# Optimization experiments

Hardware: AMD Instinct MI355X
Metric: run time of the kernel (lower is better)

The kernel has to match this reference:

```python
import jax, jax.numpy as jnp
import numpy as np
from jax.ops import segment_sum

N = 100000   # total nodes
M = 50000    # propagated subset size (len(index))
E = 600000   # edges over the subset graph
D = 128      # embedding_size
EPS = 1e-8
N_LAYERS = 3  # self.LayerNums


def setup_inputs() -> dict:
    key = jax.random.key(0)
    ks = jax.random.split(key, 12)
    features = jax.random.normal(ks[0], (N, D), dtype=jnp.float32)
    index = jnp.arange(M, dtype=jnp.int64)  # subset of nodes that get propagated
    edge_row = jax.random.randint(ks[1], (E,), 0, M, dtype=jnp.int64)
    edge_col = jax.random.randint(ks[2], (E,), 0, M, dtype=jnp.int64)
    edge_val = jax.random.uniform(ks[3], (E,), dtype=jnp.float32)
    # MLP prediction weights: D -> D//2 -> D//4 -> D//6 -> 1 (last no bias)
    def xavier(k, fan_in, fan_out):
        lim = jnp.sqrt(6.0 / (fan_in + fan_out)).astype(jnp.float32)
        return jax.random.uniform(k, (fan_in, fan_out), jnp.float32, -lim, lim)
    W1 = xavier(ks[4], D, D // 2); b1 = jnp.zeros((D // 2,), jnp.float32)
    W2 = xavier(ks[5], D // 2, D // 4); b2 = jnp.zeros((D // 4,), jnp.float32)
    W3 = xavier(ks[6], D // 4, D // 6); b3 = jnp.zeros((D // 6,), jnp.float32)
    W4 = xavier(ks[7], D // 6, 1)
    return {"features": features, "index": index, "edge_row": edge_row,
            "edge_col": edge_col, "edge_val": edge_val,
            "W1": W1, "b1": b1, "W2": W2, "b2": b2, "W3": W3, "b3": b3, "W4": W4}


def _gcn_layer(features, index, row, col, val):
    # symmetric normalization: d = rowsum(A)+eps; A' = d^-1/2 A d^-1/2
    deg = segment_sum(val, row, num_segments=M)
    d_inv_sqrt = jax.lax.rsqrt(deg + EPS)
    nval = val * d_inv_sqrt[row] * d_inv_sqrt[col]
    sub = features[index]                      # [M, D] subset_features
    msg = sub[col] * nval[:, None]             # [E, D]
    out = segment_sum(msg, row, num_segments=M)  # spmm -> [M, D]
    # new_features[index] = out; untouched rows keep original features
    return features.at[index].set(out)


def reference(features, index, edge_row, edge_col, edge_val,
              W1, b1, W2, b2, W3, b3, W4):
    x = features
    for _ in range(N_LAYERS):
        x = _gcn_layer(x, index, edge_row, edge_col, edge_val)
    # MLP prediction head (eval mode: dropout off), LeakyReLU slope 0.01
    h = jax.nn.leaky_relu(x @ W1 + b1, 0.01)
    h = jax.nn.leaky_relu(h @ W2 + b2, 0.01)
    h = jax.nn.leaky_relu(h @ W3 + b3, 0.01)
    return jax.nn.sigmoid(h @ W4)              # [N, 1]
```

## Files before the change

kernel.cpp:

```cpp
#include <hip/hip_runtime.h>
#include <math.h>

#define NN 100000
#define MM 50000
#define EE 600000
#define DD 128
#define NB 196
#define NNP 100096
#define EE4 750000

typedef short bf16x8 __attribute__((ext_vector_type(8)));
typedef float f32x4 __attribute__((ext_vector_type(4)));

__device__ __forceinline__ float bl(unsigned u) { return __uint_as_float(u << 16); }
__device__ __forceinline__ float bh(unsigned u) { return __uint_as_float(u & 0xFFFF0000u); }
__device__ __forceinline__ unsigned rne(float f) {
    unsigned u = __float_as_uint(f);
    return (u + 0x7FFFu + ((u >> 16) & 1u)) >> 16;
}
__device__ __forceinline__ unsigned pk2(float a, float b) { return rne(a) | (rne(b) << 16); }

__device__ __forceinline__ void fma21(float h, const float* wrow, float* a) {
    #pragma unroll
    for (int j = 0; j < 21; ++j) a[j] = fmaf(h, wrow[j], a[j]);
}

__global__ __launch_bounds__(256) void front_kernel(
    const int* __restrict__ row, const float* __restrict__ val,
    unsigned long long* __restrict__ dcpack, int* __restrict__ slot,
    const float* __restrict__ feat, const int* __restrict__ index,
    unsigned* __restrict__ X0b, unsigned* __restrict__ Xfull,
    const float* __restrict__ W1, const float* __restrict__ W2,
    unsigned* __restrict__ W1b, unsigned* __restrict__ W2b) {
    int i = blockIdx.x * 256 + threadIdx.x;
    int n = i >> 6, u = i & 63;
    {
        float2 f = ((const float2*)feat)[(size_t)n * 64 + u];
        Xfull[(size_t)n * 64 + u] = pk2(f.x, f.y);
    }
    if (i < MM * 64) {
        int idx = index[n];
        float2 f = ((const float2*)feat)[(size_t)idx * 64 + u];
        X0b[((size_t)(u >> 4) * MM + n) * 16 + (u & 15)] = pk2(f.x, f.y);
    }
    if (i < 4096) {
        int j = i >> 6, kp = i & 63;
        W1b[i] = pk2(W1[(2 * kp) * 64 + j], W1[(2 * kp + 1) * 64 + j]);
    } else if (i < 5120) {
        int t = i - 4096;
        int j = t >> 5, kp = t & 31;
        W2b[t] = pk2(W2[(2 * kp) * 32 + j], W2[(2 * kp + 1) * 32 + j]);
    }
    if (i < EE) {
        int r = row[i];
        unsigned long long add = (1ULL << 44) | (unsigned long long)(val[i] * 4294967296.0f);
        unsigned long long old = atomicAdd(&dcpack[r], add);
        slot[i] = (int)(old >> 44);
    }
}

__global__ void setup_kernel(const unsigned long long* __restrict__ dcpack,
                             float* __restrict__ dis, int* __restrict__ cnt,
                             int* __restrict__ blockhist) {
    __shared__ int lh[256];
    int tid = threadIdx.x;
    int i = blockIdx.x * 256 + tid;
    lh[tid] = 0;
    __syncthreads();
    if (i < MM) {
        unsigned long long pkv = dcpack[i];
        int v = (int)(pkv >> 44);
        float dsum = (float)(pkv & ((1ULL << 44) - 1)) * (1.0f / 4294967296.0f);
        dis[i] = rsqrtf(dsum + 1e-8f);
        cnt[i] = v;
        atomicAdd(&lh[min(v, 255)], 1);
    }
    __syncthreads();
    blockhist[tid * NB + blockIdx.x] = lh[tid];
}

__global__ void scan_kernel(const int* __restrict__ blockhist,
                            int* __restrict__ blockoff, int* __restrict__ total) {
    int d = blockIdx.x;
    int lane = threadIdx.x;
    int carry = 0;
    for (int base = 0; base < NB; base += 64) {
        int b = base + lane;
        int v = (b < NB) ? blockhist[d * NB + b] : 0;
        int x = v;
        #pragma unroll
        for (int off = 1; off < 64; off <<= 1) {
            int t = __shfl_up(x, off, 64);
            if (lane >= off) x += t;
        }
        if (b < NB) blockoff[d * NB + b] = carry + x - v;
        carry += __shfl(x, 63);
    }
    if (lane == 0) total[d] = carry;
}

__global__ void sort_kernel(const int* __restrict__ cnt, const int* __restrict__ blockoff,
                            const int* __restrict__ total, const int* __restrict__ index,
                            int4* __restrict__ meta, int* __restrict__ row_s4,
                            int2* __restrict__ cv_s) {
    __shared__ int lh[256], sbin[256], spad[256], ws[8];
    int tid = threadIdx.x, lane = tid & 63, w = tid >> 6;
    lh[tid] = 0;
    int t = total[tid];
    int v1 = t, v2 = t * ((tid + 3) & ~3);
    int x1 = v1, x2 = v2;
    #pragma unroll
    for (int off = 1; off < 64; off <<= 1) {
        int t1 = __shfl_up(x1, off, 64);
        int t2 = __shfl_up(x2, off, 64);
        if (lane >= off) { x1 += t1; x2 += t2; }
    }
    if (lane == 63) { ws[w] = x1; ws[4 + w] = x2; }
    __syncthreads();
    int a1 = 0, a2 = 0;
    for (int q = 0; q < w; ++q) { a1 += ws[q]; a2 += ws[4 + q]; }
    sbin[tid] = a1 + x1 - v1;
    spad[tid] = a2 + x2 - v2;
    __syncthreads();
    int i = blockIdx.x * 256 + tid;
    if (i < MM) {
        int d = cnt[i], c = min(d, 255);
        int lrank = atomicAdd(&lh[c], 1);
        int k = blockoff[c * NB + blockIdx.x] + lrank;
        int spos = sbin[c] + k;
        int s4 = spad[c] + k * ((d + 3) & ~3);
        meta[MM - 1 - spos] = make_int4(s4, d, i, index[i]);
        row_s4[i] = s4;
        int p4 = (d + 3) & ~3;
        for (int pp = d; pp < p4; ++pp) cv_s[s4 + pp] = make_int2(0, 0);
    }
}

__global__ void scatter_kernel(const int* __restrict__ row, const int* __restrict__ col,
                               const float* __restrict__ val, const float* __restrict__ dis,
                               const int* __restrict__ row_s4, const int* __restrict__ slot,
                               int2* __restrict__ cv_s) {
    int e = blockIdx.x * 256 + threadIdx.x;
    if (e < EE) {
        int r = row[e], c = col[e];
        int pos = row_s4[r] + slot[e];
        cv_s[pos] = make_int2(c, __float_as_int(val[e] * dis[r] * dis[c]));
    }
}

template <int TAG>
__global__ __launch_bounds__(256) void spmmq_kernel(
    const int4* __restrict__ meta, const int2* __restrict__ cv,
    const unsigned* __restrict__ X, unsigned* __restrict__ Y, int last) {
    int b = blockIdx.x;
    int xcd = b & 7;
    int q = xcd >> 1;
    int vb = ((b >> 3) << 1) + (xcd & 1);
    if (vb >= (MM + 15) / 16) return;
    int lane = threadIdx.x & 63, wid = threadIdx.x >> 6;
    int g = lane >> 4, sub = lane & 15;
    int ri = vb * 16 + wid * 4 + g;
    bool valid = (ri < MM);
    int rc = valid ? ri : (MM - 1);
    int4 mt = meta[rc];
    int s = mt.x, d = mt.y;
    const uint4* __restrict__ CV = (const uint4*)cv;
    const unsigned* __restrict__ Xq = X + (size_t)q * (MM * 16);
    float a0 = 0.f, a1 = 0.f;
    int e4 = s + d;
    for (int base = s; base < e4; base += 4) {
        uint4 p0 = CV[(base >> 1)];
        uint4 p1 = CV[(base >> 1) + 1];
        unsigned u0 = Xq[(int)p0.x * 16 + sub];
        unsigned u1 = Xq[(int)p0.z * 16 + sub];
        unsigned u2 = Xq[(int)p1.x * 16 + sub];
        unsigned u3 = Xq[(int)p1.z * 16 + sub];
        float v0 = __uint_as_float(p0.y), v1 = __uint_as_float(p0.w);
        float v2 = __uint_as_float(p1.y), v3 = __uint_as_float(p1.w);
        a0 = fmaf(v0, bl(u0), a0); a1 = fmaf(v0, bh(u0), a1);
        a0 = fmaf(v1, bl(u1), a0); a1 = fmaf(v1, bh(u1), a1);
        a0 = fmaf(v2, bl(u2), a0); a1 = fmaf(v2, bh(u2), a1);
        a0 = fmaf(v3, bl(u3), a0); a1 = fmaf(v3, bh(u3), a1);
    }
    if (valid) {
        unsigned o = pk2(a0, a1);
        if (last) Y[(size_t)mt.w * 64 + q * 16 + sub] = o;
        else      Y[(size_t)q * (MM * 16) + (size_t)mt.z * 16 + sub] = o;
    }
}

__global__ __launch_bounds__(256) void mlp_kernel(
    const unsigned* __restrict__ Xfull,
    const unsigned* __restrict__ W1b, const float* __restrict__ b1,
    const unsigned* __restrict__ W2b, const float* __restrict__ b2,
    const float* __restrict__ W3, const float* __restrict__ b3,
    const float* __restrict__ W4, float* __restrict__ out) {
    __shared__ float hls[4 * 1088];
    int tid = threadIdx.x;
    int lane = tid & 63, w = tid >> 6;
    int p = lane & 15, q = lane >> 4;
    float* hw = hls + w * 1088;
    int nb = blockIdx.x * 64;
    int node = nb + w * 16 + p;

    bf16x8 af[4];
    #pragma unroll
    for (int kc = 0; kc < 4; ++kc) {
        uint4 u = *(const uint4*)(Xfull + (size_t)node * 64 + kc * 16 + q * 4);
        af[kc] = *(const bf16x8*)&u;
    }
    f32x4 acc[4];
    #pragma unroll
    for (int jt = 0; jt < 4; ++jt) {
        float bv = b1[jt * 16 + p];
        acc[jt][0] = bv; acc[jt][1] = bv; acc[jt][2] = bv; acc[jt][3] = bv;
    }
    #pragma unroll
    for (int jt = 0; jt < 4; ++jt) {
        #pragma unroll
        for (int kc = 0; kc < 4; ++kc) {
            uint4 u = *(const uint4*)(W1b + (jt * 16 + p) * 64 + kc * 16 + q * 4);
            bf16x8 bf = *(const bf16x8*)&u;
            acc[jt] = __builtin_amdgcn_mfma_f32_16x16x32_bf16(af[kc], bf, acc[jt], 0, 0, 0);
        }
    }
    #pragma unroll
    for (int jt = 0; jt < 4; ++jt) {
        #pragma unroll
        for (int r = 0; r < 4; ++r) {
            float v = acc[jt][r];
            v = v > 0.f ? v : 0.01f * v;
            hw[(q * 4 + r) * 68 + jt * 16 + p] = v;
        }
    }
    bf16x8 a2f[2];
    #pragma unroll
    for (int kc = 0; kc < 2; ++kc) {
        const float* hp = hw + p * 68 + kc * 32 + q * 8;
        f32x4 v0 = *(const f32x4*)hp;
        f32x4 v1 = *(const f32x4*)(hp + 4);
        uint4 uu = make_uint4(pk2(v0[0], v0[1]), pk2(v0[2], v0[3]),
                              pk2(v1[0], v1[1]), pk2(v1[2], v1[3]));
        a2f[kc] = *(const bf16x8*)&uu;
    }
    f32x4 acc2[2];
    #pragma unroll
    for (int jt = 0; jt < 2; ++jt) {
        float bv = b2[jt * 16 + p];
        acc2[jt][0] = bv; acc2[jt][1] = bv; acc2[jt][2] = bv; acc2[jt][3] = bv;
        #pragma unroll
        for (int kc = 0; kc < 2; ++kc) {
            uint4 u = *(const uint4*)(W2b + (jt * 16 + p) * 32 + kc * 16 + q * 4);
            bf16x8 bf = *(const bf16x8*)&u;
            acc2[jt] = __builtin_amdgcn_mfma_f32_16x16x32_bf16(a2f[kc], bf, acc2[jt], 0, 0, 0);
        }
    }
    #pragma unroll
    for (int jt = 0; jt < 2; ++jt) {
        #pragma unroll
        for (int r = 0; r < 4; ++r) {
            float v = acc2[jt][r];
            v = v > 0.f ? v : 0.01f * v;
            hw[(q * 4 + r) * 36 + jt * 16 + p] = v;
        }
    }
    float a3[21];
    #pragma unroll
    for (int j = 0; j < 21; ++j) a3[j] = b3[j];
    #pragma unroll 4
    for (int k = 0; k < 32; ++k) {
        float hk = hw[p * 36 + k];
        fma21(hk, W3 + k * 21, a3);
    }
    float s = 0.f;
    #pragma unroll
    for (int j = 0; j < 21; ++j) {
        float vj = a3[j] > 0.f ? a3[j] : 0.01f * a3[j];
        s = fmaf(vj, W4[j], s);
    }
    if (q == 0) {
        int n = nb + w * 16 + p;
        if (n < NN) out[n] = 1.f / (1.f + expf(-s));
    }
}

extern "C" void kernel_launch(void* const* d_in, const int* in_sizes, int n_in,
                              void* d_out, int out_size, void* d_ws, size_t ws_size,
                              hipStream_t stream) {
    const float* feat = (const float*)d_in[0];
    const int*   index = (const int*)d_in[1];
    const int*   erow = (const int*)d_in[2];
    const int*   ecol = (const int*)d_in[3];
    const float* evalp = (const float*)d_in[4];
    const float* W1 = (const float*)d_in[5];
    const float* b1 = (const float*)d_in[6];
    const float* W2 = (const float*)d_in[7];
    const float* b2 = (const float*)d_in[8];
    const float* W3 = (const float*)d_in[9];
    const float* b3 = (const float*)d_in[10];
    const float* W4 = (const float*)d_in[11];
    float* out = (float*)d_out;

    char* ws = (char*)d_ws;
    size_t off = 0;
    auto alloc = [&](size_t bytes) -> void* {
        void* p = ws + off;
        off += (bytes + 255) & ~(size_t)255;
        return p;
    };
    unsigned long long* dcpack = (unsigned long long*)alloc((size_t)MM * 8);
    int2*  cv_s    = (int2*) alloc((size_t)EE4 * 8);
    float* dis     = (float*)alloc((size_t)MM * 4);
    int*   cnt     = (int*)  alloc((size_t)MM * 4);
    int*   slot    = (int*)  alloc((size_t)EE * 4);
    int*   row_s4  = (int*)  alloc((size_t)MM * 4);
    int*   blockhist = (int*)alloc((size_t)256 * NB * 4);
    int*   blockoff  = (int*)alloc((size_t)256 * NB * 4);
    int*   total     = (int*)alloc((size_t)256 * 4);
    int4*  meta      = (int4*)alloc((size_t)MM * 16);
    unsigned* W1b  = (unsigned*)alloc(4096 * 4);
    unsigned* W2b  = (unsigned*)alloc(1024 * 4);
    unsigned*       X0b   = (unsigned*)      alloc((size_t)MM * DD * 2);
    unsigned*       Xa    = (unsigned*)      alloc((size_t)MM * DD * 2);
    unsigned*       Xb    = (unsigned*)      alloc((size_t)MM * DD * 2);
    unsigned*       Xfull = (unsigned*)      alloc((size_t)NNP * DD * 2);

    hipMemsetAsync(dcpack, 0, (size_t)MM * 8, stream);

    front_kernel<<<(NN * 64) / 256, 256, 0, stream>>>(
        erow, evalp, dcpack, slot, feat, index, X0b, Xfull, W1, W2, W1b, W2b);
    setup_kernel<<<NB, 256, 0, stream>>>(dcpack, dis, cnt, blockhist);
    scan_kernel<<<256, 64, 0, stream>>>(blockhist, blockoff, total);
    sort_kernel<<<NB, 256, 0, stream>>>(cnt, blockoff, total, index, meta, row_s4, cv_s);
    scatter_kernel<<<(EE + 255) / 256, 256, 0, stream>>>(erow, ecol, evalp, dis,
                                                         row_s4, slot, cv_s);

    const int NGRID = (((MM + 15) / 16 + 1) / 2) * 8 + 8;
    spmmq_kernel<0><<<NGRID, 256, 0, stream>>>(meta, cv_s, X0b, Xa, 0);
    spmmq_kernel<1><<<NGRID, 256, 0, stream>>>(meta, cv_s, Xa, Xb, 0);
    spmmq_kernel<2><<<NGRID, 256, 0, stream>>>(meta, cv_s, Xb, Xfull, 1);

    mlp_kernel<<<(NNP + 63) / 64, 256, 0, stream>>>(Xfull, W1b, b1, W2b, b2,
                                                    W3, b3, W4, out);
}
```

Baseline: 273.6 us.

## Drop full-feature bf16 copy, split SpMM into per-quarter launches, gather via inverse index

Removes the Xfull bf16 copy of all N nodes. The MLP now reads propagated rows from the final quarter-split buffer through an inverse-index map, and untouched rows straight from fp32 features. Each SpMM layer is split into four launches, one per 32-column quarter, replacing the XCD-based block remapping so each launch's gather set stays cache-resident. Edge and output accesses use nontemporal loads and stores. This trades fewer bytes in the front kernel for 12 SpMM launches instead of 3 and a divergent gather path in the MLP.

```diff
diff --git a/kernel.cpp b/kernel.cpp
--- a/kernel.cpp
+++ b/kernel.cpp
@@ -11,6 +11,7 @@
 
 typedef short bf16x8 __attribute__((ext_vector_type(8)));
 typedef float f32x4 __attribute__((ext_vector_type(4)));
+typedef unsigned u32x4 __attribute__((ext_vector_type(4)));
 
 __device__ __forceinline__ float bl(unsigned u) { return __uint_as_float(u << 16); }
 __device__ __forceinline__ float bh(unsigned u) { return __uint_as_float(u & 0xFFFF0000u); }
@@ -26,23 +27,22 @@
 }
 
 __global__ __launch_bounds__(256) void front_kernel(
-    const int* __restrict__ row, const float* __restrict__ val,
+    const int* __restrict__ erow, const float* __restrict__ eval,
     unsigned long long* __restrict__ dcpack, int* __restrict__ slot,
     const float* __restrict__ feat, const int* __restrict__ index,
-    unsigned* __restrict__ X0b, unsigned* __restrict__ Xfull,
+    int* __restrict__ invidx1, unsigned* __restrict__ X0q,
     const float* __restrict__ W1, const float* __restrict__ W2,
     unsigned* __restrict__ W1b, unsigned* __restrict__ W2b) {
     int i = blockIdx.x * 256 + threadIdx.x;
-    int n = i >> 6, u = i & 63;
+    int n = i >> 5, u = i & 31;
     {
-        float2 f = ((const float2*)feat)[(size_t)n * 64 + u];
-        Xfull[(size_t)n * 64 + u] = pk2(f.x, f.y);
-    }
-    if (i < MM * 64) {
         int idx = index[n];
-        float2 f = ((const float2*)feat)[(size_t)idx * 64 + u];
-        X0b[((size_t)(u >> 4) * MM + n) * 16 + (u & 15)] = pk2(f.x, f.y);
-    }
+        float4 f = ((const float4*)feat)[(size_t)idx * 32 + u];
+        unsigned* dst = X0q + (size_t)(u >> 3) * (MM * 16) + n * 16 + ((2 * u) & 15);
+        dst[0] = pk2(f.x, f.y);
+        dst[1] = pk2(f.z, f.w);
+    }
+    if (i < MM) invidx1[index[i]] = i + 1;
     if (i < 4096) {
         int j = i >> 6, kp = i & 63;
         W1b[i] = pk2(W1[(2 * kp) * 64 + j], W1[(2 * kp + 1) * 64 + j]);
@@ -52,8 +52,8 @@
         W2b[t] = pk2(W2[(2 * kp) * 32 + j], W2[(2 * kp + 1) * 32 + j]);
     }
     if (i < EE) {
-        int r = row[i];
-        unsigned long long add = (1ULL << 44) | (unsigned long long)(val[i] * 4294967296.0f);
+        int r = erow[i];
+        unsigned long long add = (1ULL << 44) | (unsigned long long)(eval[i] * 4294967296.0f);
         unsigned long long old = atomicAdd(&dcpack[r], add);
         slot[i] = (int)(old >> 44);
     }
@@ -100,7 +100,7 @@
 }
 
 __global__ void sort_kernel(const int* __restrict__ cnt, const int* __restrict__ blockoff,
-                            const int* __restrict__ total, const int* __restrict__ index,
+                            const int* __restrict__ total,
                             int4* __restrict__ meta, int* __restrict__ row_s4,
                             int2* __restrict__ cv_s) {
     __shared__ int lh[256], sbin[256], spad[256], ws[8];
@@ -129,7 +129,7 @@
         int k = blockoff[c * NB + blockIdx.x] + lrank;
         int spos = sbin[c] + k;
         int s4 = spad[c] + k * ((d + 3) & ~3);
-        meta[MM - 1 - spos] = make_int4(s4, d, i, index[i]);
+        meta[MM - 1 - spos] = make_int4(s4, d, i, 0);
         row_s4[i] = s4;
         int p4 = (d + 3) & ~3;
         for (int pp = d; pp < p4; ++pp) cv_s[s4 + pp] = make_int2(0, 0);
@@ -148,29 +148,22 @@
     }
 }
 
-template <int TAG>
 __global__ __launch_bounds__(256) void spmmq_kernel(
     const int4* __restrict__ meta, const int2* __restrict__ cv,
-    const unsigned* __restrict__ X, unsigned* __restrict__ Y, int last) {
-    int b = blockIdx.x;
-    int xcd = b & 7;
-    int q = xcd >> 1;
-    int vb = ((b >> 3) << 1) + (xcd & 1);
-    if (vb >= (MM + 15) / 16) return;
+    const unsigned* __restrict__ Xq, unsigned* __restrict__ Yq) {
     int lane = threadIdx.x & 63, wid = threadIdx.x >> 6;
     int g = lane >> 4, sub = lane & 15;
-    int ri = vb * 16 + wid * 4 + g;
+    int ri = blockIdx.x * 16 + wid * 4 + g;
     bool valid = (ri < MM);
     int rc = valid ? ri : (MM - 1);
     int4 mt = meta[rc];
     int s = mt.x, d = mt.y;
-    const uint4* __restrict__ CV = (const uint4*)cv;
-    const unsigned* __restrict__ Xq = X + (size_t)q * (MM * 16);
+    const u32x4* __restrict__ CV = (const u32x4*)cv;
     float a0 = 0.f, a1 = 0.f;
     int e4 = s + d;
     for (int base = s; base < e4; base += 4) {
-        uint4 p0 = CV[(base >> 1)];
-        uint4 p1 = CV[(base >> 1) + 1];
+        u32x4 p0 = __builtin_nontemporal_load(CV + (base >> 1));
+        u32x4 p1 = __builtin_nontemporal_load(CV + (base >> 1) + 1);
         unsigned u0 = Xq[(int)p0.x * 16 + sub];
         unsigned u1 = Xq[(int)p0.z * 16 + sub];
         unsigned u2 = Xq[(int)p1.x * 16 + sub];
@@ -183,14 +176,13 @@
         a0 = fmaf(v3, bl(u3), a0); a1 = fmaf(v3, bh(u3), a1);
     }
     if (valid) {
-        unsigned o = pk2(a0, a1);
-        if (last) Y[(size_t)mt.w * 64 + q * 16 + sub] = o;
-        else      Y[(size_t)q * (MM * 16) + (size_t)mt.z * 16 + sub] = o;
+        __builtin_nontemporal_store(pk2(a0, a1), Yq + mt.z * 16 + sub);
     }
 }
 
 __global__ __launch_bounds__(256) void mlp_kernel(
-    const unsigned* __restrict__ Xfull,
+    const unsigned* __restrict__ Xc, const float* __restrict__ feat,
+    const int* __restrict__ invidx1,
     const unsigned* __restrict__ W1b, const float* __restrict__ b1,
     const unsigned* __restrict__ W2b, const float* __restrict__ b2,
     const float* __restrict__ W3, const float* __restrict__ b3,
@@ -202,12 +194,27 @@
     float* hw = hls + w * 1088;
     int nb = blockIdx.x * 64;
     int node = nb + w * 16 + p;
+    int nc = min(node, NN - 1);
+    int iv = invidx1[nc];
 
     bf16x8 af[4];
-    #pragma unroll
-    for (int kc = 0; kc < 4; ++kc) {
-        uint4 u = *(const uint4*)(Xfull + (size_t)node * 64 + kc * 16 + q * 4);
-        af[kc] = *(const bf16x8*)&u;
+    if (iv > 0) {
+        int r = iv - 1;
+        #pragma unroll
+        for (int kc = 0; kc < 4; ++kc) {
+            uint4 u = *(const uint4*)(Xc + (size_t)kc * (MM * 16) + r * 16 + q * 4);
+            af[kc] = *(const bf16x8*)&u;
+        }
+    } else {
+        const float4* F = (const float4*)feat;
+        #pragma unroll
+        for (int kc = 0; kc < 4; ++kc) {
+            float4 f0 = F[(size_t)nc * 32 + kc * 8 + q * 2];
+            float4 f1 = F[(size_t)nc * 32 + kc * 8 + q * 2 + 1];
+            uint4 uu = make_uint4(pk2(f0.x, f0.y), pk2(f0.z, f0.w),
+                                  pk2(f1.x, f1.y), pk2(f1.z, f1.w));
+            af[kc] = *(const bf16x8*)&uu;
+        }
     }
     f32x4 acc[4];
     #pragma unroll
@@ -279,8 +286,7 @@
         s = fmaf(vj, W4[j], s);
     }
     if (q == 0) {
-        int n = nb + w * 16 + p;
-        if (n < NN) out[n] = 1.f / (1.f + expf(-s));
+        if (node < NN) out[node] = 1.f / (1.f + expf(-s));
     }
 }
 
@@ -309,6 +315,9 @@
         return p;
     };
     unsigned long long* dcpack = (unsigned long long*)alloc((size_t)MM * 8);
+    int*   invidx1 = (int*)  alloc((size_t)NN * 4);
+    size_t zero_span = (size_t)((char*)invidx1 - (char*)dcpack) + (size_t)NN * 4;
+
     int2*  cv_s    = (int2*) alloc((size_t)EE4 * 8);
     float* dis     = (float*)alloc((size_t)MM * 4);
     int*   cnt     = (int*)  alloc((size_t)MM * 4);
@@ -320,26 +329,35 @@
     int4*  meta      = (int4*)alloc((size_t)MM * 16);
     unsigned* W1b  = (unsigned*)alloc(4096 * 4);
     unsigned* W2b  = (unsigned*)alloc(1024 * 4);
-    unsigned*       X0b   = (unsigned*)      alloc((size_t)MM * DD * 2);
-    unsigned*       Xa    = (unsigned*)      alloc((size_t)MM * DD * 2);
-    unsigned*       Xb    = (unsigned*)      alloc((size_t)MM * DD * 2);
-    unsigned*       Xfull = (unsigned*)      alloc((size_t)NNP * DD * 2);
-
-    hipMemsetAsync(dcpack, 0, (size_t)MM * 8, stream);
-
-    front_kernel<<<(NN * 64) / 256, 256, 0, stream>>>(
-        erow, evalp, dcpack, slot, feat, index, X0b, Xfull, W1, W2, W1b, W2b);
+    unsigned* X0q  = (unsigned*)alloc((size_t)MM * DD * 2);
+    unsigned* Xa   = (unsigned*)alloc((size_t)MM * DD * 2);
+    unsigned* Xb   = (unsigned*)alloc((size_t)MM * DD * 2);
+    unsigned* Xc   = (unsigned*)alloc((size_t)MM * DD * 2);
+
+    (void)hipMemsetAsync(dcpack, 0, zero_span, stream);
+
+    front_kernel<<<(MM * 32) / 256, 256, 0, stream>>>(
+        erow, evalp, dcpack, slot, feat, index, invidx1, X0q, W1, W2, W1b, W2b);
     setup_kernel<<<NB, 256, 0, stream>>>(dcpack, dis, cnt, blockhist);
     scan_kernel<<<256, 64, 0, stream>>>(blockhist, blockoff, total);
-    sort_kernel<<<NB, 256, 0, stream>>>(cnt, blockoff, total, index, meta, row_s4, cv_s);
+    sort_kernel<<<NB, 256, 0, stream>>>(cnt, blockoff, total, meta, row_s4, cv_s);
     scatter_kernel<<<(EE + 255) / 256, 256, 0, stream>>>(erow, ecol, evalp, dis,
                                                          row_s4, slot, cv_s);
 
-    const int NGRID = (((MM + 15) / 16 + 1) / 2) * 8 + 8;
-    spmmq_kernel<0><<<NGRID, 256, 0, stream>>>(meta, cv_s, X0b, Xa, 0);
-    spmmq_kernel<1><<<NGRID, 256, 0, stream>>>(meta, cv_s, Xa, Xb, 0);
-    spmmq_kernel<2><<<NGRID, 256, 0, stream>>>(meta, cv_s, Xb, Xfull, 1);
-
-    mlp_kernel<<<(NNP + 63) / 64, 256, 0, stream>>>(Xfull, W1b, b1, W2b, b2,
+    const int QSTRIDE = MM * 16;
+    const int SPGRID = (MM + 15) / 16;
+    unsigned* bufs[4] = { X0q, Xa, Xb, Xc };
+    for (int layer = 0; layer < 3; ++layer) {
+        const unsigned* Xs = bufs[layer];
+        unsigned* Yd = bufs[layer + 1];
+        for (int q = 0; q < 4; ++q) {
+            spmmq_kernel<<<SPGRID, 256, 0, stream>>>(meta, cv_s,
+                                                     Xs + (size_t)q * QSTRIDE,
+                                                     Yd + (size_t)q * QSTRIDE);
+        }
+    }
+
+    mlp_kernel<<<(NNP + 63) / 64, 256, 0, stream>>>(Xc, feat, invidx1,
+                                                    W1b, b1, W2b, b2,
                                                     W3, b3, W4, out);
 }
```

After: 334.2 us. 22.2% more time.
